# Optimization experiments

Hardware: AMD Instinct MI355X
Metric: run time of the kernel (lower is better)

## Reference

```python
import jax, jax.numpy as jnp
import numpy as np

B, LQ, LK, D = 4, 2048, 2048, 1024
H = 16  # num_heads == num_kv_heads (only runnable config of the source module)
HD = D // H  # 64


def setup_inputs() -> dict:
    key = jax.random.key(0)
    ks = jax.random.split(key, 4)
    std = 0.02
    return {
        "x": jax.random.normal(ks[0], (B, LQ, D), dtype=jnp.float32),
        "text_input": jax.random.normal(ks[1], (B, LK, D), dtype=jnp.float32),
        "Wq": jax.random.normal(ks[2], (D, D), dtype=jnp.float32) * std,
        "bq": jnp.zeros((D,), dtype=jnp.float32),
        "Wkv": jax.random.normal(ks[3], (D, 2 * D), dtype=jnp.float32) * std,
        "bkv": jnp.zeros((2 * D,), dtype=jnp.float32),
    }


def reference(x, text_input, Wq, bq, Wkv, bkv):
    b, lq, d = x.shape
    lk = text_input.shape[1]
    # projections
    Q = x @ Wq + bq                       # [b, lq, d]
    KV = text_input @ Wkv + bkv           # [b, lk, 2d]
    K, V = jnp.split(KV, 2, axis=-1)      # [b, lk, d] each
    # split heads (num_kv_heads == num_heads, so repeat_interleave is identity)
    Q = Q.reshape(b, lq, H, HD)
    K = K.reshape(b, lk, H, HD)
    V = V.reshape(b, lk, H, HD)
    # scaled dot-product attention
    scale = 1.0 / jnp.sqrt(jnp.asarray(HD, dtype=Q.dtype))
    scores = jnp.einsum("bqhd,bkhd->bhqk", Q, K) * scale  # [b, H, lq, lk]
    attn = jax.nn.softmax(scores, axis=-1)
    out = jnp.einsum("bhqk,bkhd->bqhd", attn, V)          # [b, lq, H, HD]
    # dropout p=0.0 (eval) -> identity
    return out.reshape(b, lq, d)
```

## Files before the change

kernel.cpp:

```cpp
#include <hip/hip_runtime.h>
#include <hip/hip_bf16.h>


typedef unsigned short u16;
typedef unsigned int u32;

typedef __attribute__((ext_vector_type(8))) __bf16 bf16x8;
typedef __attribute__((ext_vector_type(2))) _Float16 f16x2;
typedef __attribute__((ext_vector_type(8))) _Float16 f16x8;
typedef __attribute__((ext_vector_type(4))) float f32x4;
typedef __attribute__((ext_vector_type(16))) float f32x16;
typedef __attribute__((ext_vector_type(4))) float f4;
typedef __attribute__((ext_vector_type(4))) unsigned short u16x4;
typedef __attribute__((ext_vector_type(4))) unsigned int u32x4;

#define DEVI __device__ __forceinline__

DEVI u16 f2b(float f) {
  u32 u = __float_as_uint(f);
  return (u16)((u + 0x7fffu + ((u >> 16) & 1u)) >> 16);
}

DEVI u16 f2h(float f) {
  _Float16 h = (_Float16)f;
  return __builtin_bit_cast(u16, h);
}

DEVI f16x2 pk_f16(float a, float b) {
  return __builtin_bit_cast(f16x2, __builtin_amdgcn_cvt_pkrtz(a, b));
}

DEVI u32 cvt_pk_bf16(float a, float b) {
  u32 r;
  asm("v_cvt_pk_bf16_f32 %0, %1, %2" : "=v"(r) : "v"(a), "v"(b));
  return r;
}

DEVI void gld_lds16(void* lds, const void* g) {
  __builtin_amdgcn_global_load_lds(
      (const __attribute__((address_space(1))) u32*)g,
      (__attribute__((address_space(3))) u32*)lds, 16, 0, 0);
}

__global__ __launch_bounds__(256) void k_prep(
    const float* __restrict__ Wq, const float* __restrict__ Wkv,
    u16* __restrict__ WQT, u16* __restrict__ WKVT) {
  __shared__ float tile[32][33];
  const int bid = blockIdx.x, tid = threadIdx.x;
  const float* in;
  u16* out;
  int N, bx, by;
  if (bid < 1024) {
    in = Wq; out = WQT; N = 1024; bx = bid & 31; by = bid >> 5;
  } else {
    int b2 = bid - 1024; in = Wkv; out = WKVT; N = 2048; bx = b2 & 63; by = b2 >> 6;
  }
  const int K = 1024;
  const int n0 = bx * 32, k0 = by * 32;
  const int tx = tid & 31, ty = tid >> 5;
#pragma unroll
  for (int j = 0; j < 32; j += 8)
    tile[ty + j][tx] = in[(size_t)(k0 + ty + j) * N + n0 + tx];
  __syncthreads();
#pragma unroll
  for (int j = 0; j < 32; j += 8)
    out[(size_t)(n0 + ty + j) * K + k0 + tx] = f2b(tile[tx][ty + j]);
}

__global__ __launch_bounds__(256) void k_gemm(
    const float* __restrict__ X, const float* __restrict__ TXT,
    const u16* __restrict__ WQT, const u16* __restrict__ WKVT,
    const float* __restrict__ bq, const float* __restrict__ bkv,
    u16* __restrict__ QG, u16* __restrict__ KG, u16* __restrict__ VG) {
  __shared__ alignas(16) char As[2][8192];
  __shared__ alignas(16) char Bs[4][8192];
  const int bid0 = blockIdx.x;
  const int bid = (bid0 & 7) * 192 + (bid0 >> 3);
  const int tid = threadIdx.x;
  const int w = tid >> 6, l = tid & 63;
  const int wr = w >> 1, wc = w & 1;

  const bool isQ = bid < 512;
  int nb, mb;
  const float* Af32;
  const u16* Bptr;
  const float* bias;
  if (isQ) {
    nb = bid & 7; mb = bid >> 3; Af32 = X; Bptr = WQT; bias = bq;
  } else {
    int b2 = bid - 512; nb = b2 & 15; mb = b2 >> 4; Af32 = TXT; Bptr = WKVT; bias = bkv;
  }
  const int m0 = mb << 7, n0 = nb << 7;

  u32 doff[2], bsoff[2], fsoff[2];
#pragma unroll
  for (int i = 0; i < 2; i++) {
    u32 o = (u32)(i * 4096 + tid * 16);
    u32 row = o >> 6;
    u32 csw = (o & 63) ^ (((row >> 1) & 3) << 4);
    doff[i] = o;
    bsoff[i] = row * 2048 + csw;
    fsoff[i] = row * 4096 + 2 * csw;
  }
  const char* Abase = (const char*)Af32 + (size_t)m0 * 4096;
  const char* Borig = (const char*)Bptr + (size_t)n0 * 2048;

  f32x16 acc[2][2];
#pragma unroll
  for (int i = 0; i < 2; i++)
#pragma unroll
    for (int j = 0; j < 2; j++)
#pragma unroll
      for (int e = 0; e < 16; e++) acc[i][j][e] = 0.f;

  const u32 xk = (u32)((l >> 1) & 3);
  const u32 hi5 = (u32)(l >> 5);
  const u32 arow0 = (u32)(wr * 64 + (l & 31)) * 64;
  const u32 brow0 = (u32)(wc * 64 + (l & 31)) * 64;

  f4 sa0[2][2], sa1[2][2];

#pragma unroll
  for (int i = 0; i < 2; i++) gld_lds16(&Bs[0][doff[i]], Borig + bsoff[i]);
#pragma unroll
  for (int i = 0; i < 2; i++) {
    sa0[0][i] = *(const f4*)(Abase + fsoff[i]);
    sa1[0][i] = *(const f4*)(Abase + fsoff[i] + 16);
  }
#pragma unroll
  for (int i = 0; i < 2; i++) gld_lds16(&Bs[1][doff[i]], Borig + 64 + bsoff[i]);
#pragma unroll
  for (int i = 0; i < 2; i++) {
    sa0[1][i] = *(const f4*)(Abase + 128 + fsoff[i]);
    sa1[1][i] = *(const f4*)(Abase + 128 + fsoff[i] + 16);
  }
#pragma unroll
  for (int i = 0; i < 2; i++) {
    u32x4 pk;
    pk.x = cvt_pk_bf16(sa0[0][i].x, sa0[0][i].y);
    pk.y = cvt_pk_bf16(sa0[0][i].z, sa0[0][i].w);
    pk.z = cvt_pk_bf16(sa1[0][i].x, sa1[0][i].y);
    pk.w = cvt_pk_bf16(sa1[0][i].z, sa1[0][i].w);
    *(u32x4*)&As[0][doff[i]] = pk;
  }
  asm volatile("s_waitcnt lgkmcnt(0)" ::: "memory");
  __builtin_amdgcn_s_barrier();

#define GEMM_BODY(KT, J, P)                                                        \
  do {                                                                             \
    const int kt = (KT);                                                           \
    if (kt < 30) {                                                                 \
      _Pragma("unroll") for (int i = 0; i < 2; i++)                                \
          gld_lds16(&Bs[((J) + 2) & 3][doff[i]],                                   \
                    Borig + (u32)(kt + 2) * 64 + bsoff[i]);                        \
      _Pragma("unroll") for (int i = 0; i < 2; i++) {                              \
        sa0[(P)][i] = *(const f4*)(Abase + (u32)(kt + 2) * 128 + fsoff[i]);        \
        sa1[(P)][i] = *(const f4*)(Abase + (u32)(kt + 2) * 128 + fsoff[i] + 16);   \
      }                                                                            \
    }                                                                              \
    if (kt < 31) {                      \
      _Pragma("unroll") for (int i = 0; i < 2; i++) {                              \
        u32x4 pk;                                                                  \
        pk.x = cvt_pk_bf16(sa0[(P) ^ 1][i].x, sa0[(P) ^ 1][i].y);                  \
        pk.y = cvt_pk_bf16(sa0[(P) ^ 1][i].z, sa0[(P) ^ 1][i].w);                  \
        pk.z = cvt_pk_bf16(sa1[(P) ^ 1][i].x, sa1[(P) ^ 1][i].y);                  \
        pk.w = cvt_pk_bf16(sa1[(P) ^ 1][i].z, sa1[(P) ^ 1][i].w);                  \
        *(u32x4*)&As[(P) ^ 1][doff[i]] = pk;                                       \
      }                                                                            \
    }                                                                              \
    bf16x8 af[2][2], bfr[2][2];                                                    \
    _Pragma("unroll") for (int i = 0; i < 2; i++)                                  \
        _Pragma("unroll") for (int h = 0; h < 2; h++) {                            \
      const u32 co = (((u32)(2 * h) + hi5) ^ xk) << 4;                             \
      af[i][h] = *(const bf16x8*)&As[(P)][arow0 + (u32)i * 2048 + co];             \
      bfr[i][h] = *(const bf16x8*)&Bs[(J)][brow0 + (u32)i * 2048 + co];            \
    }                                                                              \
    _Pragma("unroll") for (int i = 0; i < 2; i++)                                  \
        _Pragma("unroll") for (int j2 = 0; j2 < 2; j2++)                           \
            _Pragma("unroll") for (int h = 0; h < 2; h++)                          \
                acc[i][j2] = __builtin_amdgcn_mfma_f32_32x32x16_bf16(              \
                    af[i][h], bfr[j2][h], acc[i][j2], 0, 0, 0);                    \
    asm volatile("s_waitcnt lgkmcnt(0)" ::: "memory");                             \
    __builtin_amdgcn_s_barrier();                                                  \
  } while (0)

  for (int k4 = 0; k4 < 8; k4++) {
    const int kt0 = k4 * 4;
    GEMM_BODY(kt0 + 0, 0, 0);
    GEMM_BODY(kt0 + 1, 1, 1);
    GEMM_BODY(kt0 + 2, 2, 0);
    GEMM_BODY(kt0 + 3, 3, 1);
  }
#undef GEMM_BODY

#pragma unroll
  for (int i = 0; i < 2; i++)
#pragma unroll
    for (int j = 0; j < 2; j++) {
      const int n = n0 + wc * 64 + j * 32 + (l & 31);
      const float bv = bias[n];
#pragma unroll
      for (int rg = 0; rg < 4; rg++) {
        const int mbase = m0 + wr * 64 + i * 32 + rg * 8 + ((l >> 5) << 2);
        const int bb = mbase >> 11;
        const int mrow = mbase & 2047;
        float a0 = acc[i][j][rg * 4 + 0] + bv;
        float a1 = acc[i][j][rg * 4 + 1] + bv;
        float a2 = acc[i][j][rg * 4 + 2] + bv;
        float a3 = acc[i][j][rg * 4 + 3] + bv;
        if (isQ) {
          const int h = n >> 6, hd = n & 63;
          u16* dst = QG + ((((size_t)bb * 16 + h) * 2048 + mrow) << 6) + hd;
          dst[0] = f2b(a0 * 0.18033688011112042f);
          dst[64] = f2b(a1 * 0.18033688011112042f);
          dst[128] = f2b(a2 * 0.18033688011112042f);
          dst[192] = f2b(a3 * 0.18033688011112042f);
        } else if (n < 1024) {
          const int h = n >> 6, d = n & 63;
          char* base = (char*)KG + ((((size_t)bb * 16 + h) * 2048 + mrow) << 7);
          float av[4] = {a0, a1, a2, a3};
#pragma unroll
          for (int r = 0; r < 4; r++) {
            u32 off = (u32)r * 128 + (((u32)d * 2) ^ (((u32)(mrow + r) & 7) << 4));
            *(u16*)(base + off) = f2b(av[r]);
          }
        } else {
          const int nn = n - 1024;
          const int h = nn >> 6, hd = nn & 63;
          u16x4 pk;
          pk.x = f2h(a0); pk.y = f2h(a1); pk.z = f2h(a2); pk.w = f2h(a3);
          char* base = (char*)VG + (((size_t)bb * 16 + h) << 18);
          u32 off = ((u32)(mrow >> 6) << 13) + (((u32)(mrow >> 5) & 1) << 12) +
                    ((u32)(hd >> 4) << 10) + (((u32)(mrow >> 2) & 3) << 8) +
                    ((u32)(hd & 15) << 4) + (((u32)(mrow >> 4) & 1) << 3);
          *(u16x4*)(base + off) = pk;
        }
      }
    }
}

__global__ __launch_bounds__(256) void k_attn(
    const u16* __restrict__ QG, const u16* __restrict__ KG, const u16* __restrict__ VG,
    float* __restrict__ out) {
  __shared__ alignas(16) char Ks[2][8192];
  __shared__ alignas(16) char Vs[2][8192];
  const int tid = threadIdx.x, w = tid >> 6, l = tid & 63;
  const int g = l >> 4, q = l & 15;
  const int bid = blockIdx.x;
  const int orig = (bid & 7) * 128 + (bid >> 3);
  const int qt = orig & 15;
  const int hh = (orig >> 4) & 15;
  const int b = orig >> 8;
  const size_t bh = (size_t)b * 16 + hh;

  const int qrowA = qt * 128 + w * 16 + q;
  const int qrowB = qrowA + 64;

  const u16* QpA = QG + ((bh * 2048 + (size_t)qrowA) << 6) + (g << 3);
  const u16* QpB = QG + ((bh * 2048 + (size_t)qrowB) << 6) + (g << 3);
  const bf16x8 qf0a = *(const bf16x8*)QpA;
  const bf16x8 qf1a = *(const bf16x8*)(QpA + 32);
  const bf16x8 qf0b = *(const bf16x8*)QpB;
  const bf16x8 qf1b = *(const bf16x8*)(QpB + 32);

  const char* Kbase = (const char*)KG + (bh << 18);
  const char* Vbase = (const char*)VG + (bh << 18);

  f32x4 lsA = (f32x4){0.f, 0.f, 0.f, 0.f};
  f32x4 lsB = (f32x4){0.f, 0.f, 0.f, 0.f};
  f32x4 oa[4], ob4[4];
#pragma unroll
  for (int c = 0; c < 4; c++) {
    oa[c] = (f32x4){0.f, 0.f, 0.f, 0.f};
    ob4[c] = (f32x4){0.f, 0.f, 0.f, 0.f};
  }
  f16x8 ones8;
#pragma unroll
  for (int e = 0; e < 8; e++) ones8[e] = (_Float16)1.0f;

  gld_lds16(&Ks[0][tid * 16], Kbase + tid * 16);
  gld_lds16(&Ks[0][4096 + tid * 16], Kbase + 4096 + tid * 16);
  gld_lds16(&Vs[0][tid * 16], Vbase + tid * 16);
  gld_lds16(&Vs[0][4096 + tid * 16], Vbase + 4096 + tid * 16);
  __syncthreads();

  const u32 ksw = ((u32)(l & 7)) << 4;
  const u32 kro = ((u32)q) << 7;
  const u32 kin = ((u32)g) << 4;

  auto body = [&](int BUF, int kb) {
    if (kb < 31) {
      const char* kp = Kbase + (size_t)(kb + 1) * 8192 + tid * 16;
      const char* vp = Vbase + (size_t)(kb + 1) * 8192 + tid * 16;
      gld_lds16(&Ks[BUF ^ 1][tid * 16], kp);
      gld_lds16(&Ks[BUF ^ 1][4096 + tid * 16], kp + 4096);
      gld_lds16(&Vs[BUF ^ 1][tid * 16], vp);
      gld_lds16(&Vs[BUF ^ 1][4096 + tid * 16], vp + 4096);
    }
    f32x4 sa[4], sb[4];
    __builtin_amdgcn_s_setprio(1);
#pragma unroll
    for (int t = 0; t < 4; t++) {
      const char* kr = &Ks[BUF][kro + (u32)t * 2048];
      bf16x8 kf0 = *(const bf16x8*)(kr + (kin ^ ksw));
      bf16x8 kf1 = *(const bf16x8*)(kr + ((kin + 64) ^ ksw));
      f32x4 z = (f32x4){0.f, 0.f, 0.f, 0.f};
      sa[t] = __builtin_amdgcn_mfma_f32_16x16x32_bf16(kf0, qf0a, z, 0, 0, 0);
      sa[t] = __builtin_amdgcn_mfma_f32_16x16x32_bf16(kf1, qf1a, sa[t], 0, 0, 0);
      sb[t] = __builtin_amdgcn_mfma_f32_16x16x32_bf16(kf0, qf0b, z, 0, 0, 0);
      sb[t] = __builtin_amdgcn_mfma_f32_16x16x32_bf16(kf1, qf1b, sb[t], 0, 0, 0);
    }
    __builtin_amdgcn_s_setprio(0);

    float pA[4][4], pB[4][4];
#pragma unroll
    for (int t = 0; t < 4; t++)
#pragma unroll
      for (int r = 0; r < 4; r++) {
        pA[t][r] = __builtin_amdgcn_exp2f(sa[t][r]);
        pB[t][r] = __builtin_amdgcn_exp2f(sb[t][r]);
      }

    __builtin_amdgcn_s_setprio(1);
#pragma unroll
    for (int u = 0; u < 2; u++) {
      f16x2 a0 = pk_f16(pA[2 * u][0], pA[2 * u][1]);
      f16x2 a1 = pk_f16(pA[2 * u][2], pA[2 * u][3]);
      f16x2 a2 = pk_f16(pA[2 * u + 1][0], pA[2 * u + 1][1]);
      f16x2 a3 = pk_f16(pA[2 * u + 1][2], pA[2 * u + 1][3]);
      f16x8 pfa;
      pfa[0] = a0.x; pfa[1] = a0.y; pfa[2] = a1.x; pfa[3] = a1.y;
      pfa[4] = a2.x; pfa[5] = a2.y; pfa[6] = a3.x; pfa[7] = a3.y;
      f16x2 b0 = pk_f16(pB[2 * u][0], pB[2 * u][1]);
      f16x2 b1 = pk_f16(pB[2 * u][2], pB[2 * u][3]);
      f16x2 b2 = pk_f16(pB[2 * u + 1][0], pB[2 * u + 1][1]);
      f16x2 b3 = pk_f16(pB[2 * u + 1][2], pB[2 * u + 1][3]);
      f16x8 pfb;
      pfb[0] = b0.x; pfb[1] = b0.y; pfb[2] = b1.x; pfb[3] = b1.y;
      pfb[4] = b2.x; pfb[5] = b2.y; pfb[6] = b3.x; pfb[7] = b3.y;
      lsA = __builtin_amdgcn_mfma_f32_16x16x32_f16(ones8, pfa, lsA, 0, 0, 0);
      lsB = __builtin_amdgcn_mfma_f32_16x16x32_f16(ones8, pfb, lsB, 0, 0, 0);
#pragma unroll
      for (int c = 0; c < 4; c++) {
        f16x8 vf = *(const f16x8*)&Vs[BUF][(u32)u * 4096 + (u32)c * 1024 + (u32)l * 16];
        oa[c] = __builtin_amdgcn_mfma_f32_16x16x32_f16(vf, pfa, oa[c], 0, 0, 0);
        ob4[c] = __builtin_amdgcn_mfma_f32_16x16x32_f16(vf, pfb, ob4[c], 0, 0, 0);
      }
    }
    __builtin_amdgcn_s_setprio(0);
    __syncthreads();
  };

  for (int kb2 = 0; kb2 < 16; kb2++) {
    body(0, 2 * kb2);
    body(1, 2 * kb2 + 1);
  }

  const float invA = 1.0f / lsA.x;
  const float invB = 1.0f / lsB.x;
  float* obA = out + ((size_t)b * 2048 + (size_t)qrowA) * 1024 + hh * 64;
  float* obB = out + ((size_t)b * 2048 + (size_t)qrowB) * 1024 + hh * 64;
#pragma unroll
  for (int c = 0; c < 4; c++) {
    f32x4 va = oa[c] * invA;
    f32x4 vb2 = ob4[c] * invB;
    *(f32x4*)(obA + c * 16 + g * 4) = va;
    *(f32x4*)(obB + c * 16 + g * 4) = vb2;
  }
}

extern "C" void kernel_launch(void* const* d_in, const int* in_sizes, int n_in,
                              void* d_out, int out_size, void* d_ws, size_t ws_size,
                              hipStream_t stream) {
  const float* x = (const float*)d_in[0];
  const float* text = (const float*)d_in[1];
  const float* Wq = (const float*)d_in[2];
  const float* bq = (const float*)d_in[3];
  const float* Wkv = (const float*)d_in[4];
  const float* bkv = (const float*)d_in[5];
  float* out = (float*)d_out;
  char* ws = (char*)d_ws;

  const size_t MiB = 1u << 20;
  u16* WQT = (u16*)(ws + 0 * MiB);
  u16* WKVT = (u16*)(ws + 2 * MiB);
  u16* QG = (u16*)(ws + 6 * MiB);
  u16* KG = (u16*)(ws + 22 * MiB);
  u16* VG = (u16*)(ws + 38 * MiB);

  k_prep<<<3072, 256, 0, stream>>>(Wq, Wkv, WQT, WKVT);
  k_gemm<<<1536, 256, 0, stream>>>(x, text, WQT, WKVT, bq, bkv, QG, KG, VG);
  k_attn<<<1024, 256, 0, stream>>>(QG, KG, VG, out);
}
```

Baseline: 163.2 us.

## Restructure projection GEMM pipeline to double-buffered B with explicit vmcnt waits

Cuts the B-tile LDS ring from four buffers to two and prefetches B one tile ahead instead of two, with an explicit vmcnt(4) wait so the direct-to-LDS loads complete before the barrier. Sched barriers pin the order of global loads, conversion stores and MFMAs, and the last iterations are peeled out of the loop. The goal is lower LDS use for better occupancy and tighter control over load/compute overlap. The risk is that the shallower B prefetch exposes more global-load latency, and that the hand-counted vmcnt values must match the actual number of outstanding loads.

```diff
diff --git a/kernel.cpp b/kernel.cpp
--- a/kernel.cpp
+++ b/kernel.cpp
@@ -73,7 +73,7 @@
     const float* __restrict__ bq, const float* __restrict__ bkv,
     u16* __restrict__ QG, u16* __restrict__ KG, u16* __restrict__ VG) {
   __shared__ alignas(16) char As[2][8192];
-  __shared__ alignas(16) char Bs[4][8192];
+  __shared__ alignas(16) char Bs[2][8192];
   const int bid0 = blockIdx.x;
   const int bid = (bid0 & 7) * 192 + (bid0 >> 3);
   const int tid = threadIdx.x;
@@ -122,13 +122,12 @@
 
 #pragma unroll
   for (int i = 0; i < 2; i++) gld_lds16(&Bs[0][doff[i]], Borig + bsoff[i]);
+  __builtin_amdgcn_sched_barrier(0);
 #pragma unroll
   for (int i = 0; i < 2; i++) {
     sa0[0][i] = *(const f4*)(Abase + fsoff[i]);
     sa1[0][i] = *(const f4*)(Abase + fsoff[i] + 16);
   }
-#pragma unroll
-  for (int i = 0; i < 2; i++) gld_lds16(&Bs[1][doff[i]], Borig + 64 + bsoff[i]);
 #pragma unroll
   for (int i = 0; i < 2; i++) {
     sa0[1][i] = *(const f4*)(Abase + 128 + fsoff[i]);
@@ -143,55 +142,75 @@
     pk.w = cvt_pk_bf16(sa1[0][i].z, sa1[0][i].w);
     *(u32x4*)&As[0][doff[i]] = pk;
   }
-  asm volatile("s_waitcnt lgkmcnt(0)" ::: "memory");
+  __builtin_amdgcn_sched_barrier(0);
+  asm volatile("s_waitcnt vmcnt(4) lgkmcnt(0)" ::: "memory");
   __builtin_amdgcn_s_barrier();
 
-#define GEMM_BODY(KT, J, P)                                                        \
+#define GEMM_MFMA(BUF)                                                             \
   do {                                                                             \
-    const int kt = (KT);                                                           \
-    if (kt < 30) {                                                                 \
-      _Pragma("unroll") for (int i = 0; i < 2; i++)                                \
-          gld_lds16(&Bs[((J) + 2) & 3][doff[i]],                                   \
-                    Borig + (u32)(kt + 2) * 64 + bsoff[i]);                        \
-      _Pragma("unroll") for (int i = 0; i < 2; i++) {                              \
-        sa0[(P)][i] = *(const f4*)(Abase + (u32)(kt + 2) * 128 + fsoff[i]);        \
-        sa1[(P)][i] = *(const f4*)(Abase + (u32)(kt + 2) * 128 + fsoff[i] + 16);   \
-      }                                                                            \
-    }                                                                              \
-    if (kt < 31) {                      \
-      _Pragma("unroll") for (int i = 0; i < 2; i++) {                              \
-        u32x4 pk;                                                                  \
-        pk.x = cvt_pk_bf16(sa0[(P) ^ 1][i].x, sa0[(P) ^ 1][i].y);                  \
-        pk.y = cvt_pk_bf16(sa0[(P) ^ 1][i].z, sa0[(P) ^ 1][i].w);                  \
-        pk.z = cvt_pk_bf16(sa1[(P) ^ 1][i].x, sa1[(P) ^ 1][i].y);                  \
-        pk.w = cvt_pk_bf16(sa1[(P) ^ 1][i].z, sa1[(P) ^ 1][i].w);                  \
-        *(u32x4*)&As[(P) ^ 1][doff[i]] = pk;                                       \
-      }                                                                            \
-    }                                                                              \
     bf16x8 af[2][2], bfr[2][2];                                                    \
     _Pragma("unroll") for (int i = 0; i < 2; i++)                                  \
         _Pragma("unroll") for (int h = 0; h < 2; h++) {                            \
       const u32 co = (((u32)(2 * h) + hi5) ^ xk) << 4;                             \
-      af[i][h] = *(const bf16x8*)&As[(P)][arow0 + (u32)i * 2048 + co];             \
-      bfr[i][h] = *(const bf16x8*)&Bs[(J)][brow0 + (u32)i * 2048 + co];            \
+      af[i][h] = *(const bf16x8*)&As[(BUF)][arow0 + (u32)i * 2048 + co];           \
+      bfr[i][h] = *(const bf16x8*)&Bs[(BUF)][brow0 + (u32)i * 2048 + co];          \
     }                                                                              \
     _Pragma("unroll") for (int i = 0; i < 2; i++)                                  \
         _Pragma("unroll") for (int j2 = 0; j2 < 2; j2++)                           \
             _Pragma("unroll") for (int h = 0; h < 2; h++)                          \
                 acc[i][j2] = __builtin_amdgcn_mfma_f32_32x32x16_bf16(              \
                     af[i][h], bfr[j2][h], acc[i][j2], 0, 0, 0);                    \
-    asm volatile("s_waitcnt lgkmcnt(0)" ::: "memory");                             \
+  } while (0)
+
+#define GEMM_CVT(SET, DSTBUF)                                                      \
+  do {                                                                             \
+    _Pragma("unroll") for (int i = 0; i < 2; i++) {                                \
+      u32x4 pk;                                                                    \
+      pk.x = cvt_pk_bf16(sa0[(SET)][i].x, sa0[(SET)][i].y);                        \
+      pk.y = cvt_pk_bf16(sa0[(SET)][i].z, sa0[(SET)][i].w);                        \
+      pk.z = cvt_pk_bf16(sa1[(SET)][i].x, sa1[(SET)][i].y);                        \
+      pk.w = cvt_pk_bf16(sa1[(SET)][i].z, sa1[(SET)][i].w);                        \
+      *(u32x4*)&As[(DSTBUF)][doff[i]] = pk;                                        \
+    }                                                                              \
+  } while (0)
+
+#define GEMM_BODY(KT, BUF)                                                         \
+  do {                                                                             \
+    const int kt = (KT);                                                           \
+    _Pragma("unroll") for (int i = 0; i < 2; i++)       \
+        gld_lds16(&Bs[(BUF) ^ 1][doff[i]], Borig + (u32)(kt + 1) * 64 + bsoff[i]); \
+    __builtin_amdgcn_sched_barrier(0);                                             \
+    _Pragma("unroll") for (int i = 0; i < 2; i++) {        \
+      sa0[(BUF)][i] = *(const f4*)(Abase + (u32)(kt + 2) * 128 + fsoff[i]);        \
+      sa1[(BUF)][i] = *(const f4*)(Abase + (u32)(kt + 2) * 128 + fsoff[i] + 16);   \
+    }                                                                              \
+    GEMM_CVT((BUF) ^ 1, (BUF) ^ 1);      \
+    GEMM_MFMA(BUF);                                                                \
+    __builtin_amdgcn_sched_barrier(0);                                             \
+    asm volatile("s_waitcnt vmcnt(4) lgkmcnt(0)" ::: "memory");                    \
     __builtin_amdgcn_s_barrier();                                                  \
   } while (0)
 
-  for (int k4 = 0; k4 < 8; k4++) {
-    const int kt0 = k4 * 4;
-    GEMM_BODY(kt0 + 0, 0, 0);
-    GEMM_BODY(kt0 + 1, 1, 1);
-    GEMM_BODY(kt0 + 2, 2, 0);
-    GEMM_BODY(kt0 + 3, 3, 1);
-  }
+  for (int k2 = 0; k2 < 15; k2++) {
+    GEMM_BODY(2 * k2, 0);
+    GEMM_BODY(2 * k2 + 1, 1);
+  }
+
+#pragma unroll
+  for (int i = 0; i < 2; i++)
+    gld_lds16(&Bs[1][doff[i]], Borig + (u32)31 * 64 + bsoff[i]);
+  __builtin_amdgcn_sched_barrier(0);
+  GEMM_CVT(1, 1);
+  GEMM_MFMA(0);
+  __builtin_amdgcn_sched_barrier(0);
+  asm volatile("s_waitcnt vmcnt(0) lgkmcnt(0)" ::: "memory");
+  __builtin_amdgcn_s_barrier();
+
+  GEMM_MFMA(1);
+
 #undef GEMM_BODY
+#undef GEMM_CVT
+#undef GEMM_MFMA
 
 #pragma unroll
   for (int i = 0; i < 2; i++)
```

Measured after the change: 162.4 us. About the same (-0.5%).
